# Performance work log

Measured on AMD Instinct MI355X. Metric: run time of the kernel, lower is better.

Reference implementation:

```python
import jax, jax.numpy as jnp
import numpy as np

D = 1024      # embed_dim
E = 2048      # expand * embed_dim
S_DIM = 128   # shrunken attn dim s
C = 256       # chunk size
SRC = 4096    # src_len
G = SRC // C  # num chunks
B = 8
STD = 0.02


def setup_inputs() -> dict:
    key = jax.random.key(0)
    ks = jax.random.split(key, 16)
    n = lambda k, shp: jax.random.normal(k, shp, dtype=jnp.float32)
    inp = {
        "query": n(ks[0], (SRC, B, D)),
        "key":   n(ks[1], (SRC, B, D)),
        "value": n(ks[2], (SRC, B, D)),
        # learned params (torch Linear stored as [in, out])
        "Wxs": n(ks[3], (D, S_DIM)) * STD, "bxs": n(ks[4], (S_DIM,)) * STD,
        "Wve": n(ks[5], (D, E)) * STD,     "bve": n(ks[6], (E,)) * STD,
        "Wue": n(ks[7], (D, E)) * STD,     "bue": n(ks[8], (E,)) * STD,
        "Wod": n(ks[9], (E, D)) * STD,     "bod": n(ks[10], (D,)) * STD,
        "rel_bias": n(ks[11], (C,)) * STD,
        "gamma": n(ks[12], (4, S_DIM)) * STD,
        "beta":  n(ks[13], (4, S_DIM)) * STD,
    }
    return inp


def reference(query, key, value, Wxs, bxs, Wve, bve, Wue, bue, Wod, bod,
              rel_bias, gamma, beta):
    # [S, B, D] -> [B, G, C, D]
    x = jnp.transpose(value, (1, 0, 2)).reshape(B, G, C, D)
    v = jnp.tanh(x @ Wve + bve)          # [b,g,c,e]
    z = jnp.tanh(x @ Wxs + bxs)          # [b,g,c,s]
    q_quad = z * gamma[0] + beta[0]
    k_quad = z * gamma[1] + beta[1]
    q_lin  = z * gamma[2] + beta[2]
    k_lin  = z * gamma[3] + beta[3]
    # local quadratic attention: relu(qk + bias)^2
    qk = jnp.einsum('bgns,bgms->bgnm', q_quad, k_quad)
    a = jnp.square(jax.nn.relu(qk + rel_bias))
    v_quad = jnp.einsum('bgnm,bgme->bgne', a, v)
    # global linear attention
    kv = jnp.einsum('bgcs,bgce->bse', k_lin, v)
    v_lin = jnp.einsum('bgcs,bse->bgce', q_lin, kv)
    u = jnp.tanh(x @ Wue + bue)          # [b,g,c,e]
    o = (u * (v_quad + v_lin)) @ Wod + bod   # [b,g,c,d]
    o = o.reshape(B, G * C, D)
    return jnp.transpose(o, (1, 0, 2))   # [S, B, D]
```

## Files before the change

### kernel.cpp

```cpp
#include <hip/hip_runtime.h>
#include <hip/hip_bf16.h>

using u16 = unsigned short;
using u32 = unsigned int;

typedef __attribute__((ext_vector_type(8))) short bf8;
typedef __attribute__((ext_vector_type(4))) float f4;
typedef __attribute__((ext_vector_type(4))) u16  us4;

#define DEV static __device__ __forceinline__

DEV float bf2f(u16 u) { return __uint_as_float(((u32)u) << 16); }
DEV u16 f2bf(float f) {
    u32 x = __float_as_uint(f);
    x += 0x7FFFu + ((x >> 16) & 1u);
    return (u16)(x >> 16);
}
DEV float tanhf_fast(float x) {
    float e = __expf(2.0f * x);
    return 1.0f - 2.0f / (e + 1.0f);
}
DEV f4 MFMA(bf8 a, bf8 b, f4 c) {
    return __builtin_amdgcn_mfma_f32_16x16x32_bf16(a, b, c, 0, 0, 0);
}
DEV int xcd_swz(int bx, int nwg) { return (bx & 7) * (nwg >> 3) + (bx >> 3); }

DEV void gload16(const u16* src, u16* dst) {
    __builtin_amdgcn_global_load_lds(
        (const __attribute__((address_space(1))) void*)src,
        (__attribute__((address_space(3))) void*)dst, 16, 0, 0);
}

#define SBAR()  __builtin_amdgcn_s_barrier()
#define SCHED() __builtin_amdgcn_sched_barrier(0)


#define WS_XB    ((size_t)0)
#define WS_WXST  ((size_t)67108864)
#define WS_WVET  ((size_t)67371008)
#define WS_WUET  ((size_t)71565312)
#define WS_WODT  ((size_t)75759616)
#define WS_KVT   ((size_t)79953920)
#define WS_A     ((size_t)84148224)
#define WS_QL    ((size_t)100925440)
#define WS_VT    ((size_t)109314048)
#define WS_T1    ((size_t)243531776)
#define WS_Z     ((size_t)243531776)
#define WS_KLT   ((size_t)251920384)
#define WS_QQ    ((size_t)260308992)
#define WS_KQ    ((size_t)268697600)
#define WS_KVF   ((size_t)277086208)

DEV void stage128x64(const u16* __restrict__ gbase, int ld, u16* lds, int w, int lane) {
    const int srow = lane >> 3;
    const int scol = ((lane & 7) ^ srow) * 8;
    #pragma unroll
    for (int i = 0; i < 4; i++) {
        const int rt = (i * 4 + w) * 8 + srow;
        gload16(gbase + (size_t)rt * ld + scol, lds + (size_t)(i * 4 + w) * 512);
    }
}

DEV void frag_mfma_64_swz(const u16* As, const u16* Bs, int wm, int wn, int ln, int lh,
                          f4 acc[4][4]) {
    #pragma unroll
    for (int kk2 = 0; kk2 < 2; kk2++) {
        const int sx = (((kk2 << 2) + lh) ^ (ln & 7)) << 3;
        bf8 a[4], b[4];
        #pragma unroll
        for (int mt = 0; mt < 4; mt++)
            a[mt] = *reinterpret_cast<const bf8*>(As + (wm * 64 + mt * 16 + ln) * 64 + sx);
        #pragma unroll
        for (int nt = 0; nt < 4; nt++)
            b[nt] = *reinterpret_cast<const bf8*>(Bs + (wn * 64 + nt * 16 + ln) * 64 + sx);
        #pragma unroll
        for (int mt = 0; mt < 4; mt++)
            #pragma unroll
            for (int nt = 0; nt < 4; nt++)
                acc[mt][nt] = MFMA(a[mt], b[nt], acc[mt][nt]);
    }
}

template<int NT, typename FA, typename FB>
DEV void gemm_pipe(FA stageA, FB stageB, u16* As, u16* Bs,
                   int wm, int wn, int ln, int lh, f4 acc[4][4]) {
    stageA(As, 0); stageB(Bs, 0);
    #pragma unroll 2
    for (int t = 0; t + 1 < NT; ++t) {
        u16* An = As + ((t & 1) ^ 1) * 8192;
        u16* Bn = Bs + ((t & 1) ^ 1) * 8192;
        stageA(An, t + 1); stageB(Bn, t + 1);
        asm volatile("s_waitcnt vmcnt(8)" ::: "memory");
        SBAR(); SCHED();
        frag_mfma_64_swz(As + (t & 1) * 8192, Bs + (t & 1) * 8192, wm, wn, ln, lh, acc);
        SCHED(); SBAR(); SCHED();
    }
    asm volatile("s_waitcnt vmcnt(0)" ::: "memory");
    SBAR();
    frag_mfma_64_swz(As + ((NT - 1) & 1) * 8192, Bs + ((NT - 1) & 1) * 8192, wm, wn, ln, lh, acc);
    SBAR();
}


#define T256 16384

DEV void stage2(const u16* __restrict__ gbase, int ld, u16* lds, int tid, int i0, int i1) {
    const int slot = tid & 7;
    {
        const int row = i0 * 64 + (tid >> 3);
        gload16(gbase + (size_t)row * ld + ((slot ^ (row & 7)) << 3),
                lds + ((size_t)(i0 * 512 + (tid & ~63)) << 3));
    }
    {
        const int row = i1 * 64 + (tid >> 3);
        gload16(gbase + (size_t)row * ld + ((slot ^ (row & 7)) << 3),
                lds + ((size_t)(i1 * 512 + (tid & ~63)) << 3));
    }
}

#define RD16(p, off) (*reinterpret_cast<const bf8*>((p) + (off)))

template<int NT, typename FA, typename FB>
DEV void gemm_pipe8(FA sA, FB sB, u16* As, u16* Bs,
                    int wm, int wn, int ln, int lh, f4 acc[8][4]) {
    const u32 x7   = (u32)(ln & 7);
    const u32 swz0 = ((u32)lh ^ x7) << 4;
    const u32 swz1 = ((4u | (u32)lh) ^ x7) << 4;
    const char* a0 = (const char*)As + (u32)(wm * 128 + ln) * 128;
    const char* b0 = (const char*)Bs + (u32)(wn * 64 + ln) * 128;
    const char* pA[2][2] = {{a0 + swz0, a0 + swz1}, {a0 + 32768 + swz0, a0 + 32768 + swz1}};
    const char* pB[2][2] = {{b0 + swz0, b0 + swz1}, {b0 + 32768 + swz0, b0 + 32768 + swz1}};

    sA(As, 0, 0, 2); sA(As, 0, 1, 3); sB(Bs, 0, 0, 1); sB(Bs, 0, 2, 3);
    if (NT > 1) {
        sA(As + T256, 1, 0, 2); sA(As + T256, 1, 1, 3);
        sB(Bs + T256, 1, 0, 1); sB(Bs + T256, 1, 2, 3);
        asm volatile("s_waitcnt vmcnt(8)" ::: "memory");
    } else {
        asm volatile("s_waitcnt vmcnt(0)" ::: "memory");
    }
    SBAR(); SCHED();

    auto body = [&](int t, const int c) {
        u16* Ac = As + c * T256;
        u16* Bc = Bs + c * T256;
        const char* pa0 = pA[c][0]; const char* pa1 = pA[c][1];
        const char* pb0 = pB[c][0]; const char* pb1 = pB[c][1];
        bf8 aR[8], br0[4], br1[4];
        #pragma unroll
        for (int j = 0; j < 4; j++) {
            aR[j]     = RD16(pa0, j * 2048);
            aR[4 + j] = RD16(pa1, j * 2048);
        }
        #pragma unroll
        for (int k = 0; k < 2; k++) {
            br0[k]     = RD16(pb0, k * 2048);
            br0[2 + k] = RD16(pb1, k * 2048);
        }
        SBAR(); SCHED();
        __builtin_amdgcn_s_setprio(1);
        #pragma unroll
        for (int j = 0; j < 4; j++) { acc[j][0] = MFMA(aR[j], br0[0], acc[j][0]);
                                      acc[j][1] = MFMA(aR[j], br0[1], acc[j][1]); }
        #pragma unroll
        for (int j = 0; j < 4; j++) { acc[j][0] = MFMA(aR[4 + j], br0[2], acc[j][0]);
                                      acc[j][1] = MFMA(aR[4 + j], br0[3], acc[j][1]); }
        __builtin_amdgcn_s_setprio(0);
        SCHED();
        #pragma unroll
        for (int k = 0; k < 2; k++) {
            br1[k]     = RD16(pb0, (2 + k) * 2048);
            br1[2 + k] = RD16(pb1, (2 + k) * 2048);
        }
        SBAR(); SCHED();
        __builtin_amdgcn_s_setprio(1);
        #pragma unroll
        for (int j = 0; j < 4; j++) { acc[j][2] = MFMA(aR[j], br1[0], acc[j][2]);
                                      acc[j][3] = MFMA(aR[j], br1[1], acc[j][3]); }
        #pragma unroll
        for (int j = 0; j < 4; j++) { acc[j][2] = MFMA(aR[4 + j], br1[2], acc[j][2]);
                                      acc[j][3] = MFMA(aR[4 + j], br1[3], acc[j][3]); }
        __builtin_amdgcn_s_setprio(0);
        SCHED();
        #pragma unroll
        for (int j = 0; j < 4; j++) {
            aR[j]     = RD16(pa0, 8192 + j * 2048);
            aR[4 + j] = RD16(pa1, 8192 + j * 2048);
        }
        if (t + 2 < NT) { sA(Ac, t + 2, 0, 2); sB(Bc, t + 2, 0, 1); }
        SBAR(); SCHED();
        __builtin_amdgcn_s_setprio(1);
        #pragma unroll
        for (int j = 0; j < 4; j++) { acc[4 + j][0] = MFMA(aR[j], br0[0], acc[4 + j][0]);
                                      acc[4 + j][1] = MFMA(aR[j], br0[1], acc[4 + j][1]); }
        #pragma unroll
        for (int j = 0; j < 4; j++) { acc[4 + j][0] = MFMA(aR[4 + j], br0[2], acc[4 + j][0]);
                                      acc[4 + j][1] = MFMA(aR[4 + j], br0[3], acc[4 + j][1]); }
        __builtin_amdgcn_s_setprio(0);
        SCHED();
        if (t + 2 < NT) {
            sA(Ac, t + 2, 1, 3); sB(Bc, t + 2, 2, 3);
            asm volatile("s_waitcnt vmcnt(8)" ::: "memory");
        } else if (t + 1 < NT) {
            asm volatile("s_waitcnt vmcnt(0)" ::: "memory");
        }
        SBAR(); SCHED();
        __builtin_amdgcn_s_setprio(1);
        #pragma unroll
        for (int j = 0; j < 4; j++) { acc[4 + j][2] = MFMA(aR[j], br1[0], acc[4 + j][2]);
                                      acc[4 + j][3] = MFMA(aR[j], br1[1], acc[4 + j][3]); }
        #pragma unroll
        for (int j = 0; j < 4; j++) { acc[4 + j][2] = MFMA(aR[4 + j], br1[2], acc[4 + j][2]);
                                      acc[4 + j][3] = MFMA(aR[4 + j], br1[3], acc[4 + j][3]); }
        __builtin_amdgcn_s_setprio(0);
        SCHED();
    };
    for (int t = 0; t < NT; t += 2) {
        body(t, 0);
        body(t + 1, 1);
    }
}

__global__ void k_cvt_x(const float* __restrict__ src, u16* __restrict__ dst) {
    int m = blockIdx.x;
    int s = m >> 3, b = m & 7;
    const float* in = src + (size_t)m * 1024;
    u16* outp = dst + (((size_t)b << 12) + s) * 1024;
    int t = threadIdx.x * 4;
    float4 v = *reinterpret_cast<const float4*>(in + t);
    us4 o; o[0] = f2bf(v.x); o[1] = f2bf(v.y); o[2] = f2bf(v.z); o[3] = f2bf(v.w);
    *reinterpret_cast<us4*>(outp + t) = o;
}

__global__ void k_transpose(const float* __restrict__ src, u16* __restrict__ dst, int R, int C) {
    __shared__ u16 tile[32][33];
    int tx = threadIdx.x & 31, ty = threadIdx.x >> 5;
    int r0 = blockIdx.y * 32, c0 = blockIdx.x * 32;
    #pragma unroll
    for (int rr = ty; rr < 32; rr += 8)
        tile[rr][tx] = f2bf(src[(size_t)(r0 + rr) * C + c0 + tx]);
    __syncthreads();
    #pragma unroll
    for (int cc = ty; cc < 32; cc += 8)
        dst[(size_t)(c0 + cc) * R + r0 + tx] = tile[tx][cc];
}

__global__ void k_klinT(const u16* __restrict__ z, const float* __restrict__ gamma,
                        const float* __restrict__ beta, u16* __restrict__ klt) {
    __shared__ u16 tile[32][33];
    int tx = threadIdx.x & 31, ty = threadIdx.x >> 5;
    int r0 = blockIdx.x * 32;
    int c0 = blockIdx.y * 32;
    float gs = gamma[384 + c0 + tx], bs = beta[384 + c0 + tx];
    #pragma unroll
    for (int rr = ty; rr < 32; rr += 8) {
        u16 zv = z[(size_t)(r0 + rr) * 128 + c0 + tx];
        tile[rr][tx] = f2bf(bf2f(zv) * gs + bs);
    }
    __syncthreads();
    int b = r0 >> 12;
    int pos0 = r0 & 4095;
    #pragma unroll
    for (int cc = ty; cc < 32; cc += 8)
        klt[(((size_t)b * 128 + c0 + cc) << 12) + pos0 + tx] = tile[tx][cc];
}

__global__ __launch_bounds__(256) void k_zgemm(const u16* __restrict__ xb, const u16* __restrict__ WxsT,
                                               const float* __restrict__ bxs,
                                               const float* __restrict__ gamma, const float* __restrict__ beta,
                                               u16* __restrict__ z, u16* __restrict__ qq,
                                               u16* __restrict__ kq, u16* __restrict__ ql) {
    __shared__ u16 As[2][128 * 64];
    __shared__ u16 Bs[2][128 * 64];
    const int tid = threadIdx.x;
    const int lane = tid & 63, w = tid >> 6;
    const int ln = lane & 15, lh = lane >> 4;
    const int wm = w >> 1, wn = w & 1;
    const int rowbase = xcd_swz(blockIdx.x, 256) * 128;
    const u16* Ab = xb + (size_t)rowbase * 1024;
    f4 acc[4][4] = {};
    gemm_pipe<16>(
        [&](u16* l, int t) { stage128x64(Ab + t * 64, 1024, l, w, lane); },
        [&](u16* l, int t) { stage128x64(WxsT + t * 64, 1024, l, w, lane); },
        As[0], Bs[0], wm, wn, ln, lh, acc);
    #pragma unroll
    for (int mt = 0; mt < 4; mt++)
        #pragma unroll
        for (int nt = 0; nt < 4; nt++) {
            int col = wn * 64 + nt * 16 + ln;
            float bias = bxs[col];
            float g0 = gamma[col],       b0 = beta[col];
            float g1 = gamma[128 + col], b1 = beta[128 + col];
            float g2 = gamma[256 + col], b2 = beta[256 + col];
            int r0 = rowbase + wm * 64 + mt * 16 + lh * 4;
            #pragma unroll
            for (int rg = 0; rg < 4; rg++) {
                float zv = tanhf_fast(acc[mt][nt][rg] + bias);
                size_t idx = ((size_t)(r0 + rg) << 7) + col;
                z[idx]  = f2bf(zv);
                qq[idx] = f2bf(zv * g0 + b0);
                kq[idx] = f2bf(zv * g1 + b1);
                ql[idx] = f2bf(zv * g2 + b2);
            }
        }
}

__global__ __launch_bounds__(512, 2) void k_vgemm(const u16* __restrict__ xb, const u16* __restrict__ WveT,
                                                  const float* __restrict__ bve, u16* __restrict__ vT) {
    __shared__ u16 As[2 * T256];
    __shared__ u16 Bs[2 * T256];
    const int tid = threadIdx.x;
    const int lane = tid & 63, w = tid >> 6;
    const int ln = lane & 15, lh = lane >> 4;
    const int wm = w >> 2, wn = w & 3;
    const int rowbase = xcd_swz(blockIdx.x, 128) * 256;
    const int colbase = blockIdx.y * 256;
    const u16* Ag = xb + (size_t)rowbase * 1024;
    const u16* Bg = WveT + (size_t)colbase * 1024;
    f4 acc[8][4] = {};
    gemm_pipe8<16>(
        [&](u16* l, int t, int i0, int i1) { stage2(Ag + t * 64, 1024, l, tid, i0, i1); },
        [&](u16* l, int t, int i0, int i1) { stage2(Bg + t * 64, 1024, l, tid, i0, i1); },
        As, Bs, wm, wn, ln, lh, acc);
    #pragma unroll
    for (int mt = 0; mt < 8; mt++)
        #pragma unroll
        for (int nt = 0; nt < 4; nt++) {
            int e = colbase + wn * 64 + nt * 16 + ln;
            float bias = bve[e];
            int r0 = rowbase + wm * 128 + mt * 16 + lh * 4;
            int bb = r0 >> 12, s0 = r0 & 4095;
            us4 p;
            #pragma unroll
            for (int rg = 0; rg < 4; rg++) p[rg] = f2bf(tanhf_fast(acc[mt][nt][rg] + bias));
            *reinterpret_cast<us4*>(vT + (((size_t)bb * 2048 + e) << 12) + s0) = p;
        }
}

__global__ __launch_bounds__(256) void k_kv(const u16* __restrict__ vT, const u16* __restrict__ klt,
                                            float* __restrict__ kvF) {
    __shared__ u16 As[2][128 * 64];
    __shared__ u16 Bs[2][128 * 64];
    const int tid = threadIdx.x;
    const int lane = tid & 63, w = tid >> 6;
    const int ln = lane & 15, lh = lane >> 4;
    const int wm = w >> 1, wn = w & 1;
    const int b = blockIdx.z;
    const int rowbase = blockIdx.x * 128;
    const int kbase = blockIdx.y * 1024;
    const u16* Ab = vT + ((size_t)b * 2048 + rowbase) * 4096 + kbase;
    const u16* Bb = klt + ((size_t)b * 128) * 4096 + kbase;
    f4 acc[4][4] = {};
    gemm_pipe<16>(
        [&](u16* l, int t) { stage128x64(Ab + t * 64, 4096, l, w, lane); },
        [&](u16* l, int t) { stage128x64(Bb + t * 64, 4096, l, w, lane); },
        As[0], Bs[0], wm, wn, ln, lh, acc);
    #pragma unroll
    for (int mt = 0; mt < 4; mt++)
        #pragma unroll
        for (int nt = 0; nt < 4; nt++) {
            int s = wn * 64 + nt * 16 + ln;
            int e0 = rowbase + wm * 64 + mt * 16 + lh * 4;
            #pragma unroll
            for (int rg = 0; rg < 4; rg++)
                atomicAdd(&kvF[(((size_t)b * 2048 + e0 + rg) << 7) + s], acc[mt][nt][rg]);
        }
}

__global__ void k_kvcvt(const float* __restrict__ kvF, u16* __restrict__ kvT, int n) {
    int i = (blockIdx.x * blockDim.x + threadIdx.x) * 4;
    if (i < n) {
        float4 v = *reinterpret_cast<const float4*>(kvF + i);
        us4 o; o[0] = f2bf(v.x); o[1] = f2bf(v.y); o[2] = f2bf(v.z); o[3] = f2bf(v.w);
        *reinterpret_cast<us4*>(kvT + i) = o;
    }
}

__global__ __launch_bounds__(256) void k_a(const u16* __restrict__ qq, const u16* __restrict__ kq,
                                           const float* __restrict__ rel_bias, u16* __restrict__ a_out) {
    const int lane = threadIdx.x & 63, wid = threadIdx.x >> 6;
    const int ln = lane & 15, lh = lane >> 4;
    const int wm = wid >> 1, wn = wid & 1;
    const int ci = blockIdx.y;
    const int qbase = blockIdx.x * 128 + wm * 64;
    const int nbase = wn * 128;
    const int rowbase = ci << 8;
    f4 acc[4][8] = {};
    const u16* qr[4];
    #pragma unroll
    for (int mt = 0; mt < 4; mt++) qr[mt] = qq + ((size_t)(rowbase + qbase + mt * 16 + ln) << 7);
    const u16* kr[8];
    #pragma unroll
    for (int nt = 0; nt < 8; nt++) kr[nt] = kq + ((size_t)(rowbase + nbase + nt * 16 + ln) << 7);
    #pragma unroll
    for (int kk = 0; kk < 128; kk += 32) {
        int k0 = kk + lh * 8;
        bf8 aq[4], ak[8];
        #pragma unroll
        for (int mt = 0; mt < 4; mt++) aq[mt] = *reinterpret_cast<const bf8*>(qr[mt] + k0);
        #pragma unroll
        for (int nt = 0; nt < 8; nt++) ak[nt] = *reinterpret_cast<const bf8*>(kr[nt] + k0);
        #pragma unroll
        for (int mt = 0; mt < 4; mt++)
            #pragma unroll
            for (int nt = 0; nt < 8; nt++)
                acc[mt][nt] = MFMA(aq[mt], ak[nt], acc[mt][nt]);
    }
    #pragma unroll
    for (int nt = 0; nt < 8; nt++) {
        int key = nbase + nt * 16 + ln;
        float rb = rel_bias[key];
        #pragma unroll
        for (int mt = 0; mt < 4; mt++) {
            int r0 = qbase + mt * 16 + lh * 4;
            #pragma unroll
            for (int rg = 0; rg < 4; rg++) {
                float v = acc[mt][nt][rg] + rb;
                v = fmaxf(v, 0.0f); v = v * v;
                a_out[((size_t)ci << 16) + ((size_t)(r0 + rg) << 8) + key] = f2bf(v);
            }
        }
    }
}

__global__ __launch_bounds__(512, 2) void k_t1(const u16* __restrict__ ql, const u16* __restrict__ a_in,
                                               const u16* __restrict__ vT, const u16* __restrict__ kvT,
                                               u16* __restrict__ t1) {
    __shared__ u16 As[2 * T256];
    __shared__ u16 Bs[2 * T256];
    const int tid = threadIdx.x;
    const int lane = tid & 63, w = tid >> 6;
    const int ln = lane & 15, lh = lane >> 4;
    const int wm = w >> 2, wn = w & 3;
    const int ci = xcd_swz(blockIdx.x, 128);
    const int rowbase = ci << 8;
    const int ebase = blockIdx.y * 256;
    const int b = ci >> 4, g = ci & 15;
    const u16* Aa = ql + (size_t)rowbase * 128;
    const u16* Ba = kvT + ((size_t)(b * 2048 + ebase)) * 128;
    const u16* Ab2 = a_in + ((size_t)ci << 16);
    const u16* Bb2 = vT + ((size_t)(b * 2048 + ebase)) * 4096 + (g << 8);
    f4 acc[8][4] = {};
    gemm_pipe8<6>(
        [&](u16* l, int t, int i0, int i1) {
            if (t < 2) stage2(Aa + t * 64, 128, l, tid, i0, i1);
            else       stage2(Ab2 + (t - 2) * 64, 256, l, tid, i0, i1);
        },
        [&](u16* l, int t, int i0, int i1) {
            if (t < 2) stage2(Ba + t * 64, 128, l, tid, i0, i1);
            else       stage2(Bb2 + (t - 2) * 64, 4096, l, tid, i0, i1);
        },
        As, Bs, wm, wn, ln, lh, acc);
    #pragma unroll
    for (int mt = 0; mt < 8; mt++)
        #pragma unroll
        for (int nt = 0; nt < 4; nt++) {
            int e = ebase + wn * 64 + nt * 16 + ln;
            int r0 = rowbase + wm * 128 + mt * 16 + lh * 4;
            #pragma unroll
            for (int rg = 0; rg < 4; rg++)
                t1[((size_t)(r0 + rg) << 11) + e] = f2bf(acc[mt][nt][rg]);
        }
}

__global__ __launch_bounds__(512, 2) void k_u(const u16* __restrict__ xb, const u16* __restrict__ WueT,
                                              const float* __restrict__ bue, u16* t1) {
    __shared__ u16 As[2 * T256];
    __shared__ u16 Bs[2 * T256];
    const int tid = threadIdx.x;
    const int lane = tid & 63, w = tid >> 6;
    const int ln = lane & 15, lh = lane >> 4;
    const int wm = w >> 2, wn = w & 3;
    const int rowbase = xcd_swz(blockIdx.x, 128) * 256;
    const int colbase = blockIdx.y * 256;
    const u16* Ag = xb + (size_t)rowbase * 1024;
    const u16* Bg = WueT + (size_t)colbase * 1024;
    f4 acc[8][4] = {};
    gemm_pipe8<16>(
        [&](u16* l, int t, int i0, int i1) { stage2(Ag + t * 64, 1024, l, tid, i0, i1); },
        [&](u16* l, int t, int i0, int i1) { stage2(Bg + t * 64, 1024, l, tid, i0, i1); },
        As, Bs, wm, wn, ln, lh, acc);
    #pragma unroll
    for (int mt = 0; mt < 8; mt++)
        #pragma unroll
        for (int nt = 0; nt < 4; nt++) {
            int e = colbase + wn * 64 + nt * 16 + ln;
            float bias = bue[e];
            int r0 = rowbase + wm * 128 + mt * 16 + lh * 4;
            #pragma unroll
            for (int rg = 0; rg < 4; rg++) {
                size_t idx = ((size_t)(r0 + rg) << 11) + e;
                float t = bf2f(t1[idx]);
                float u = tanhf_fast(acc[mt][nt][rg] + bias);
                t1[idx] = f2bf(u * t);
            }
        }
}

__global__ __launch_bounds__(512, 2) void k_o(const u16* __restrict__ t1, const u16* __restrict__ WodT,
                                              const float* __restrict__ bod, float* __restrict__ out) {
    __shared__ u16 As[2 * T256];
    __shared__ u16 Bs[2 * T256];
    const int tid = threadIdx.x;
    const int lane = tid & 63, w = tid >> 6;
    const int ln = lane & 15, lh = lane >> 4;
    const int wm = w >> 2, wn = w & 3;
    const int rowbase = xcd_swz(blockIdx.x, 128) * 256;
    const int colbase = blockIdx.y * 256;
    const u16* Ag = t1 + (size_t)rowbase * 2048;
    const u16* Bg = WodT + (size_t)colbase * 2048;
    f4 acc[8][4] = {};
    gemm_pipe8<32>(
        [&](u16* l, int t, int i0, int i1) { stage2(Ag + t * 64, 2048, l, tid, i0, i1); },
        [&](u16* l, int t, int i0, int i1) { stage2(Bg + t * 64, 2048, l, tid, i0, i1); },
        As, Bs, wm, wn, ln, lh, acc);
    #pragma unroll
    for (int mt = 0; mt < 8; mt++)
        #pragma unroll
        for (int nt = 0; nt < 4; nt++) {
            int d = colbase + wn * 64 + nt * 16 + ln;
            float bias = bod[d];
            int r0 = rowbase + wm * 128 + mt * 16 + lh * 4;
            #pragma unroll
            for (int rg = 0; rg < 4; rg++) {
                int r = r0 + rg;
                int s = r & 4095, bb = r >> 12;
                out[((size_t)(s * 8 + bb) << 10) + d] = acc[mt][nt][rg] + bias;
            }
        }
}

extern "C" void kernel_launch(void* const* d_in, const int* in_sizes, int n_in,
                              void* d_out, int out_size, void* d_ws, size_t ws_size,
                              hipStream_t stream) {
    const float* value = (const float*)d_in[2];
    const float* Wxs = (const float*)d_in[3];  const float* bxs = (const float*)d_in[4];
    const float* Wve = (const float*)d_in[5];  const float* bve = (const float*)d_in[6];
    const float* Wue = (const float*)d_in[7];  const float* bue = (const float*)d_in[8];
    const float* Wod = (const float*)d_in[9];  const float* bod = (const float*)d_in[10];
    const float* rel_bias = (const float*)d_in[11];
    const float* gamma = (const float*)d_in[12];
    const float* beta  = (const float*)d_in[13];
    float* out = (float*)d_out;

    char* ws = (char*)d_ws;
    u16* xb   = (u16*)(ws + WS_XB);
    u16* WxsT = (u16*)(ws + WS_WXST);
    u16* WveT = (u16*)(ws + WS_WVET);
    u16* WueT = (u16*)(ws + WS_WUET);
    u16* WodT = (u16*)(ws + WS_WODT);
    u16* kvT  = (u16*)(ws + WS_KVT);
    u16* a    = (u16*)(ws + WS_A);
    u16* ql   = (u16*)(ws + WS_QL);
    u16* vT   = (u16*)(ws + WS_VT);
    u16* t1   = (u16*)(ws + WS_T1);
    u16* z    = (u16*)(ws + WS_Z);
    u16* klt  = (u16*)(ws + WS_KLT);
    u16* qq   = (u16*)(ws + WS_QQ);
    u16* kq   = (u16*)(ws + WS_KQ);
    float* kvF = (float*)(ws + WS_KVF);

    k_cvt_x<<<32768, 256, 0, stream>>>(value, xb);
    k_transpose<<<dim3(4, 32),  256, 0, stream>>>(Wxs, WxsT, 1024, 128);
    k_transpose<<<dim3(64, 32), 256, 0, stream>>>(Wve, WveT, 1024, 2048);
    k_transpose<<<dim3(64, 32), 256, 0, stream>>>(Wue, WueT, 1024, 2048);
    k_transpose<<<dim3(32, 64), 256, 0, stream>>>(Wod, WodT, 2048, 1024);
    k_zgemm<<<256, 256, 0, stream>>>(xb, WxsT, bxs, gamma, beta, z, qq, kq, ql);
    k_klinT<<<dim3(1024, 4), 256, 0, stream>>>(z, gamma, beta, klt);
    k_vgemm<<<dim3(128, 8), 512, 0, stream>>>(xb, WveT, bve, vT);
    hipMemsetAsync(kvF, 0, (size_t)8 * 2048 * 128 * 4, stream);
    k_kv<<<dim3(16, 4, 8), 256, 0, stream>>>(vT, klt, kvF);
    k_kvcvt<<<2048, 256, 0, stream>>>(kvF, kvT, 8 * 2048 * 128);
    k_a<<<dim3(2, 128), 256, 0, stream>>>(qq, kq, rel_bias, a);
    k_t1<<<dim3(128, 8), 512, 0, stream>>>(ql, a, vT, kvT, t1);
    k_u<<<dim3(128, 8), 512, 0, stream>>>(xb, WueT, bue, t1);
    k_o<<<dim3(128, 4), 512, 0, stream>>>(t1, WodT, bod, out);
}
```

Baseline: 760.2 us.

## Fuse t1 and u GEMMs into one kernel and co-locate tiles per XCD

Merges the t1 GEMM (linear plus quadratic attention) and the u GEMM into a single kernel that keeps the t1 accumulator in registers, applies the tanh gate and writes t1 once. This removes a full bf16 write and read-back of the [32768x2048] t1 intermediate plus one kernel launch. It also replaces the 2D grids with a 1D remap that places all column tiles of a row block on the same XCD, so the shared A rows can be reused from that XCD's L2. The cost is two accumulator sets live at once in the fused kernel, which raises register pressure and may lower occupancy.

```diff
diff --git a/kernel.cpp b/kernel.cpp
--- a/kernel.cpp
+++ b/kernel.cpp
@@ -24,6 +24,11 @@
     return __builtin_amdgcn_mfma_f32_16x16x32_bf16(a, b, c, 0, 0, 0);
 }
 DEV int xcd_swz(int bx, int nwg) { return (bx & 7) * (nwg >> 3) + (bx >> 3); }
+DEV void remap_coloc(int bid, int clog2, int rpx, int& row, int& col) {
+    int x = bid & 7, n = bid >> 3;
+    col = n & ((1 << clog2) - 1);
+    row = x * rpx + (n >> clog2);
+}
 
 DEV void gload16(const u16* src, u16* dst) {
     __builtin_amdgcn_global_load_lds(
@@ -313,8 +318,10 @@
     const int lane = tid & 63, w = tid >> 6;
     const int ln = lane & 15, lh = lane >> 4;
     const int wm = w >> 2, wn = w & 3;
-    const int rowbase = xcd_swz(blockIdx.x, 128) * 256;
-    const int colbase = blockIdx.y * 256;
+    int rowt, colt;
+    remap_coloc(blockIdx.x, 3, 16, rowt, colt);
+    const int rowbase = rowt * 256;
+    const int colbase = colt * 256;
     const u16* Ag = xb + (size_t)rowbase * 1024;
     const u16* Bg = WveT + (size_t)colbase * 1024;
     f4 acc[8][4] = {};
@@ -423,21 +430,25 @@
     }
 }
 
-__global__ __launch_bounds__(512, 2) void k_t1(const u16* __restrict__ ql, const u16* __restrict__ a_in,
-                                               const u16* __restrict__ vT, const u16* __restrict__ kvT,
-                                               u16* __restrict__ t1) {
+__global__ __launch_bounds__(512, 2) void k_t1u(const u16* __restrict__ ql, const u16* __restrict__ a_in,
+                                                const u16* __restrict__ vT, const u16* __restrict__ kvT,
+                                                const u16* __restrict__ xb, const u16* __restrict__ WueT,
+                                                const float* __restrict__ bue, u16* __restrict__ t1) {
     __shared__ u16 As[2 * T256];
     __shared__ u16 Bs[2 * T256];
     const int tid = threadIdx.x;
     const int lane = tid & 63, w = tid >> 6;
     const int ln = lane & 15, lh = lane >> 4;
     const int wm = w >> 2, wn = w & 3;
-    const int ci = xcd_swz(blockIdx.x, 128);
+    int rowt, colt;
+    remap_coloc(blockIdx.x, 3, 16, rowt, colt);
+    const int ci = rowt;
     const int rowbase = ci << 8;
-    const int ebase = blockIdx.y * 256;
+    const int ebase = colt * 256;
     const int b = ci >> 4, g = ci & 15;
-    const u16* Aa = ql + (size_t)rowbase * 128;
-    const u16* Ba = kvT + ((size_t)(b * 2048 + ebase)) * 128;
+
+    const u16* Aa  = ql + (size_t)rowbase * 128;
+    const u16* Ba  = kvT + ((size_t)(b * 2048 + ebase)) * 128;
     const u16* Ab2 = a_in + ((size_t)ci << 16);
     const u16* Bb2 = vT + ((size_t)(b * 2048 + ebase)) * 4096 + (g << 8);
     f4 acc[8][4] = {};
@@ -451,48 +462,26 @@
             else       stage2(Bb2 + (t - 2) * 64, 4096, l, tid, i0, i1);
         },
         As, Bs, wm, wn, ln, lh, acc);
-    #pragma unroll
-    for (int mt = 0; mt < 8; mt++)
-        #pragma unroll
-        for (int nt = 0; nt < 4; nt++) {
-            int e = ebase + wn * 64 + nt * 16 + ln;
-            int r0 = rowbase + wm * 128 + mt * 16 + lh * 4;
-            #pragma unroll
-            for (int rg = 0; rg < 4; rg++)
-                t1[((size_t)(r0 + rg) << 11) + e] = f2bf(acc[mt][nt][rg]);
-        }
-}
-
-__global__ __launch_bounds__(512, 2) void k_u(const u16* __restrict__ xb, const u16* __restrict__ WueT,
-                                              const float* __restrict__ bue, u16* t1) {
-    __shared__ u16 As[2 * T256];
-    __shared__ u16 Bs[2 * T256];
-    const int tid = threadIdx.x;
-    const int lane = tid & 63, w = tid >> 6;
-    const int ln = lane & 15, lh = lane >> 4;
-    const int wm = w >> 2, wn = w & 3;
-    const int rowbase = xcd_swz(blockIdx.x, 128) * 256;
-    const int colbase = blockIdx.y * 256;
+
     const u16* Ag = xb + (size_t)rowbase * 1024;
-    const u16* Bg = WueT + (size_t)colbase * 1024;
-    f4 acc[8][4] = {};
+    const u16* Bg = WueT + (size_t)ebase * 1024;
+    f4 accu[8][4] = {};
     gemm_pipe8<16>(
         [&](u16* l, int t, int i0, int i1) { stage2(Ag + t * 64, 1024, l, tid, i0, i1); },
         [&](u16* l, int t, int i0, int i1) { stage2(Bg + t * 64, 1024, l, tid, i0, i1); },
-        As, Bs, wm, wn, ln, lh, acc);
+        As, Bs, wm, wn, ln, lh, accu);
+
     #pragma unroll
     for (int mt = 0; mt < 8; mt++)
         #pragma unroll
         for (int nt = 0; nt < 4; nt++) {
-            int e = colbase + wn * 64 + nt * 16 + ln;
+            int e = ebase + wn * 64 + nt * 16 + ln;
             float bias = bue[e];
             int r0 = rowbase + wm * 128 + mt * 16 + lh * 4;
             #pragma unroll
             for (int rg = 0; rg < 4; rg++) {
-                size_t idx = ((size_t)(r0 + rg) << 11) + e;
-                float t = bf2f(t1[idx]);
-                float u = tanhf_fast(acc[mt][nt][rg] + bias);
-                t1[idx] = f2bf(u * t);
+                float uu = tanhf_fast(accu[mt][nt][rg] + bias);
+                t1[((size_t)(r0 + rg) << 11) + e] = f2bf(uu * acc[mt][nt][rg]);
             }
         }
 }
@@ -505,8 +494,10 @@
     const int lane = tid & 63, w = tid >> 6;
     const int ln = lane & 15, lh = lane >> 4;
     const int wm = w >> 2, wn = w & 3;
-    const int rowbase = xcd_swz(blockIdx.x, 128) * 256;
-    const int colbase = blockIdx.y * 256;
+    int rowt, colt;
+    remap_coloc(blockIdx.x, 2, 16, rowt, colt);
+    const int rowbase = rowt * 256;
+    const int colbase = colt * 256;
     const u16* Ag = t1 + (size_t)rowbase * 2048;
     const u16* Bg = WodT + (size_t)colbase * 2048;
     f4 acc[8][4] = {};
@@ -567,12 +558,11 @@
     k_transpose<<<dim3(32, 64), 256, 0, stream>>>(Wod, WodT, 2048, 1024);
     k_zgemm<<<256, 256, 0, stream>>>(xb, WxsT, bxs, gamma, beta, z, qq, kq, ql);
     k_klinT<<<dim3(1024, 4), 256, 0, stream>>>(z, gamma, beta, klt);
-    k_vgemm<<<dim3(128, 8), 512, 0, stream>>>(xb, WveT, bve, vT);
+    k_vgemm<<<1024, 512, 0, stream>>>(xb, WveT, bve, vT);
     hipMemsetAsync(kvF, 0, (size_t)8 * 2048 * 128 * 4, stream);
     k_kv<<<dim3(16, 4, 8), 256, 0, stream>>>(vT, klt, kvF);
     k_kvcvt<<<2048, 256, 0, stream>>>(kvF, kvT, 8 * 2048 * 128);
     k_a<<<dim3(2, 128), 256, 0, stream>>>(qq, kq, rel_bias, a);
-    k_t1<<<dim3(128, 8), 512, 0, stream>>>(ql, a, vT, kvT, t1);
-    k_u<<<dim3(128, 8), 512, 0, stream>>>(xb, WueT, bue, t1);
-    k_o<<<dim3(128, 4), 512, 0, stream>>>(t1, WodT, bod, out);
-}
+    k_t1u<<<1024, 512, 0, stream>>>(ql, a, vT, kvT, xb, WueT, bue, t1);
+    k_o<<<512, 512, 0, stream>>>(t1, WodT, bod, out);
+}
```

Result: slower. 807.1 us (+6.2%).
